# Kernel tuning notes

Measured on AMD Instinct MI355X. Metric: run time of the kernel, lower is better.

Reference implementation:

```python
import jax, jax.numpy as jnp
import numpy as np
import math

B, L, N, DIM, H = 2, 8, 1024, 512, 8
DH = DIM // H

def setup_inputs() -> dict:
    key = jax.random.key(0)
    ks = jax.random.split(key, 9)
    s = 1.0 / math.sqrt(DIM)
    return {
        "x": jax.random.normal(ks[0], (B, L, N, DIM), dtype=jnp.float32),
        "Wq": jax.random.normal(ks[1], (DIM, DIM), dtype=jnp.float32) * s,
        "bq": jnp.zeros((DIM,), dtype=jnp.float32),
        "Wk": jax.random.normal(ks[2], (DIM, DIM), dtype=jnp.float32) * s,
        "bk": jnp.zeros((DIM,), dtype=jnp.float32),
        "Wv": jax.random.normal(ks[3], (DIM, DIM), dtype=jnp.float32) * s,
        "bv": jnp.zeros((DIM,), dtype=jnp.float32),
        "Wo": jax.random.normal(ks[4], (DIM, DIM), dtype=jnp.float32) * s,
        "bo": jnp.zeros((DIM,), dtype=jnp.float32),
    }

def _split_heads(t):
    # 'b l n (h d) -> b l h n d'
    b, l, n, _ = t.shape
    return t.reshape(b, l, n, H, DH).transpose(0, 1, 3, 2, 4)

def reference(x, Wq, bq, Wk, bk, Wv, bv, Wo, bo):
    q = _split_heads(x @ Wq.T + bq)
    # FAITHFUL BUG: source maps (q, v, k) -> (q_mat, k_mat, v_mat),
    # so the "keys" come from the v projection and "values" from the k projection.
    k_mat = _split_heads(x @ Wv.T + bv)
    v_mat = _split_heads(x @ Wk.T + bk)
    # scale is sqrt(Dh * num_heads) = sqrt(dim), as in the source
    scores = jnp.einsum('blhnd,blhmd->blhnm', q, k_mat) / math.sqrt(DIM)
    weights = jax.nn.softmax(scores, axis=-1)
    inter = jnp.einsum('blhnm,blhmd->blhnd', weights, v_mat)
    # 'b l h n d -> b l n (h d)'
    inter = inter.transpose(0, 1, 3, 2, 4).reshape(x.shape[0], x.shape[1], x.shape[2], DIM)
    return inter @ Wo.T + bo
```

## Files before the change

kernel.cpp:

```cpp
#include <hip/hip_runtime.h>
#include <stdint.h>

#define DIMC 512
#define NSEQ 1024
#define BLT  16
#define NHEAD 8
#define DHD  64
#define MTOT (BLT*NSEQ)

typedef float f32x4 __attribute__((ext_vector_type(4)));
typedef short s16x8 __attribute__((ext_vector_type(8)));
typedef short s16x4 __attribute__((ext_vector_type(4)));

__device__ __forceinline__ unsigned short f2bf(float f) {
    unsigned int u = __float_as_uint(f);
    u += 0x7fffu + ((u >> 16) & 1u);
    return (unsigned short)(u >> 16);
}
__device__ __forceinline__ float bf2f(unsigned short h) {
    return __uint_as_float(((unsigned int)h) << 16);
}

#define QSCALE (0.04419417382415922f * 1.4426950408889634f)

__device__ __forceinline__ void gll16(const void* g, void* l) {
    __builtin_amdgcn_global_load_lds(
        (const __attribute__((address_space(1))) void*)g,
        (__attribute__((address_space(3))) void*)l, 16, 0, 0);
}

__device__ __forceinline__ f32x4 mfma16_bf16(s16x4 a, s16x4 b, f32x4 c) {
#if __has_builtin(__builtin_amdgcn_mfma_f32_16x16x16bf16_1k)
    return __builtin_amdgcn_mfma_f32_16x16x16bf16_1k(a, b, c, 0, 0, 0);
#else
    asm volatile("v_mfma_f32_16x16x16_bf16 %0, %1, %2, %0"
                 : "+v"(c) : "v"(a), "v"(b));
    return c;
#endif
}

__device__ __forceinline__ bool detect_bf16(const unsigned short* x) {
    int t = threadIdx.x & 63;
    unsigned short v = x[2 * t];
    int e = (v >> 7) & 0xFF;
    unsigned long long ball = __ballot(e < 100 || e > 137);
    return __popcll(ball) < 16;
}

struct ConvArgs {
    const void* src[9];
    unsigned short* dst[9];
};

__global__ __launch_bounds__(256) void conv_kernel(ConvArgs a,
                                                   const unsigned short* __restrict__ xdet) {
    const bool isbf = detect_bf16(xdet);
    int b = blockIdx.x;
    int seg, idx;
    if (b < 4096)      { seg = 0; idx = (b * 256 + threadIdx.x) * 8; }
    else if (b < 4608) { int t = b - 4096; seg = 1 + (t >> 7);
                         idx = (((t & 127) * 256) + threadIdx.x) * 8; }
    else               { int i = threadIdx.x * 8; seg = 5 + (i >> 9); idx = i & 511; }
    const void* s = a.src[seg];
    unsigned short* d = a.dst[seg];
    if (isbf) {
        *(uint4*)(d + idx) = *(const uint4*)((const unsigned short*)s + idx);
    } else {
        float4 t0 = *(const float4*)((const float*)s + idx);
        float4 t1 = *(const float4*)((const float*)s + idx + 4);
        ushort4 v0{f2bf(t0.x), f2bf(t0.y), f2bf(t0.z), f2bf(t0.w)};
        ushort4 v1{f2bf(t1.x), f2bf(t1.y), f2bf(t1.z), f2bf(t1.w)};
        *(ushort4*)(d + idx)     = v0;
        *(ushort4*)(d + idx + 4) = v1;
    }
}

__device__ __forceinline__ void gemm_core_async(
    const unsigned short* __restrict__ Ap, const unsigned short* __restrict__ Wp,
    int mBase, int nBase, unsigned short* Al, unsigned short* Bl, f32x4 acc[4][4])
{
    const int wave = threadIdx.x >> 6;
    const int lane = threadIdx.x & 63;
    const int lr = lane & 15, lg = lane >> 4;
    const int wm = wave >> 1, wn = wave & 1;
    const int srow = lane >> 3;
    const int scol = (lane & 7) * 8;

    #pragma unroll
    for (int a = 0; a < 4; ++a)
        #pragma unroll
        for (int b = 0; b < 4; ++b) acc[a][b] = (f32x4){0.f, 0.f, 0.f, 0.f};

    for (int k0 = 0; k0 < DIMC; k0 += 64) {
        #pragma unroll
        for (int i = 0; i < 4; ++i) {
            int rbase = (wave * 4 + i) * 8;
            gll16(Ap + (long)(mBase + rbase + srow) * DIMC + k0 + scol, Al + rbase * 64);
            gll16(Wp + (long)(nBase + rbase + srow) * DIMC + k0 + scol, Bl + rbase * 64);
        }
        __syncthreads();

        #pragma unroll
        for (int kk = 0; kk < 64; kk += 32) {
            s16x8 af[4], bf_[4];
            #pragma unroll
            for (int a = 0; a < 4; ++a)
                af[a] = *(const s16x8*)&Al[(wm * 64 + a * 16 + lr) * 64 + kk + lg * 8];
            #pragma unroll
            for (int b = 0; b < 4; ++b)
                bf_[b] = *(const s16x8*)&Bl[(wn * 64 + b * 16 + lr) * 64 + kk + lg * 8];
            #pragma unroll
            for (int a = 0; a < 4; ++a)
                #pragma unroll
                for (int b = 0; b < 4; ++b)
                    acc[a][b] = __builtin_amdgcn_mfma_f32_16x16x32_bf16(af[a], bf_[b], acc[a][b], 0, 0, 0);
        }
        __syncthreads();
    }
}

__global__ __launch_bounds__(256) void proj_kernel(
    const unsigned short* __restrict__ xb,
    const unsigned short* __restrict__ Wqb, const unsigned short* __restrict__ Wkb,
    const unsigned short* __restrict__ Wvb,
    const unsigned short* __restrict__ bqb, const unsigned short* __restrict__ bkb,
    const unsigned short* __restrict__ bvb,
    unsigned short* __restrict__ Q, unsigned short* __restrict__ K,
    unsigned short* __restrict__ Vt)
{
    const int z = blockIdx.z;
    const unsigned short* Wp = (z == 0) ? Wqb : ((z == 1) ? Wvb : Wkb);
    const unsigned short* bp = (z == 0) ? bqb : ((z == 1) ? bvb : bkb);
    unsigned short* outp = (z == 0) ? Q : ((z == 1) ? K : Vt);
    const float oscale = (z == 0) ? QSCALE : 1.0f;

    const int mBase = blockIdx.x * 128;
    const int nBase = blockIdx.y * 128;
    const int lane = threadIdx.x & 63;
    const int lr = lane & 15, lg = lane >> 4;
    const int wm = (threadIdx.x >> 6) >> 1, wn = (threadIdx.x >> 6) & 1;

    __shared__ unsigned short Al[128 * 64];
    __shared__ unsigned short Bl[128 * 64];
    f32x4 acc[4][4];
    gemm_core_async(xb, Wp, mBase, nBase, Al, Bl, acc);

    #pragma unroll
    for (int b = 0; b < 4; ++b) {
        int j = nBase + wn * 64 + b * 16 + lr;
        float bb = bf2f(bp[j]);
        int h = j >> 6, d = j & 63;
        #pragma unroll
        for (int a = 0; a < 4; ++a) {
            int m0 = mBase + wm * 64 + a * 16 + lg * 4;
            int bl = m0 >> 10, n0 = m0 & 1023;
            if (z == 2) {
                ushort4 pk;
                unsigned short* p = (unsigned short*)&pk;
                #pragma unroll
                for (int r = 0; r < 4; ++r) p[r] = f2bf(acc[a][b][r] + bb);
                *(ushort4*)&outp[(((bl << 3) + h) << 16) + (d << 10) + n0] = pk;
            } else {
                #pragma unroll
                for (int r = 0; r < 4; ++r) {
                    float v = (acc[a][b][r] + bb) * oscale;
                    outp[(((bl << 3) + h) << 16) + ((n0 + r) << 6) + d] = f2bf(v);
                }
            }
        }
    }
}

__global__ __launch_bounds__(256) void out_gemm_kernel(
    const unsigned short* __restrict__ inter, const unsigned short* __restrict__ Wob,
    const unsigned short* __restrict__ bob, void* __restrict__ outp,
    const unsigned short* __restrict__ xdet)
{
    const bool isbf = detect_bf16(xdet);
    const int mBase = blockIdx.x * 128;
    const int nBase = blockIdx.y * 128;
    const int lane = threadIdx.x & 63;
    const int lr = lane & 15, lg = lane >> 4;
    const int wm = (threadIdx.x >> 6) >> 1, wn = (threadIdx.x >> 6) & 1;

    __shared__ unsigned short Al[128 * 64];
    __shared__ unsigned short Bl[128 * 64];
    f32x4 acc[4][4];
    gemm_core_async(inter, Wob, mBase, nBase, Al, Bl, acc);

    #pragma unroll
    for (int b = 0; b < 4; ++b) {
        int j = nBase + wn * 64 + b * 16 + lr;
        float bb = bf2f(bob[j]);
        #pragma unroll
        for (int a = 0; a < 4; ++a) {
            #pragma unroll
            for (int r = 0; r < 4; ++r) {
                long m = mBase + wm * 64 + a * 16 + lg * 4 + r;
                float v = acc[a][b][r] + bb;
                if (isbf) ((unsigned short*)outp)[m * DIMC + j] = f2bf(v);
                else      ((float*)outp)[m * DIMC + j] = v;
            }
        }
    }
}

#define SWZ(row, col) ((row) * 64 + ((col) ^ (((row) & 7) * 8)))

__global__ __launch_bounds__(256) void attn_kernel(
    const unsigned short* __restrict__ Q, const unsigned short* __restrict__ K,
    const unsigned short* __restrict__ Vt, unsigned short* __restrict__ inter)
{
    const int inst = blockIdx.x;
    const int bh = inst >> 2;
    const int qt = inst & 3;
    const int wave = threadIdx.x >> 6;
    const int lane = threadIdx.x & 63;
    const int lr = lane & 15;
    const int lg = lane >> 4;

    const unsigned short* Qb = Q + (long)bh * (NSEQ * DHD);
    const int qbase = qt * 256 + wave * 64;

    s16x8 qf[4][2];
    #pragma unroll
    for (int g = 0; g < 4; ++g)
        #pragma unroll
        for (int kk = 0; kk < 2; ++kk)
            qf[g][kk] = *(const s16x8*)&Qb[(qbase + g * 16 + lr) * DHD + kk * 32 + lg * 8];

    __shared__ unsigned short Kl[64 * 64];
    __shared__ unsigned short Vl[64 * 64];

    f32x4 o[4][4];
    #pragma unroll
    for (int g = 0; g < 4; ++g)
        #pragma unroll
        for (int m = 0; m < 4; ++m) o[g][m] = (f32x4){0.f, 0.f, 0.f, 0.f};
    float l_acc[4] = {0.f, 0.f, 0.f, 0.f};

    for (int kt = 0; kt < 16; ++kt) {
        const unsigned short* Kb = K + (long)bh * (NSEQ * DHD) + kt * 64 * DHD;
        const unsigned short* Vb = Vt + (long)bh * (NSEQ * DHD) + kt * 64;

        #pragma unroll
        for (int i = 0; i < 2; ++i) {
            int f = threadIdx.x + 256 * i;
            int row = f >> 3, c8 = (f & 7) * 8;
            *(uint4*)&Kl[SWZ(row, c8)] = *(const uint4*)&Kb[row * DHD + c8];
            *(uint4*)&Vl[SWZ(row, c8)] = *(const uint4*)&Vb[row * NSEQ + c8];
        }
        __syncthreads();

        f32x4 s[4][4];
        #pragma unroll
        for (int g = 0; g < 4; ++g)
            #pragma unroll
            for (int c = 0; c < 4; ++c) s[g][c] = (f32x4){0.f, 0.f, 0.f, 0.f};
        #pragma unroll
        for (int kk = 0; kk < 2; ++kk) {
            s16x8 af[4];
            #pragma unroll
            for (int c = 0; c < 4; ++c)
                af[c] = *(const s16x8*)&Kl[SWZ(c * 16 + lr, kk * 32 + lg * 8)];
            #pragma unroll
            for (int g = 0; g < 4; ++g)
                #pragma unroll
                for (int c = 0; c < 4; ++c)
                    s[g][c] = __builtin_amdgcn_mfma_f32_16x16x32_bf16(af[c], qf[g][kk], s[g][c], 0, 0, 0);
        }

        s16x4 pb[4][4];
        #pragma unroll
        for (int g = 0; g < 4; ++g)
            #pragma unroll
            for (int c = 0; c < 4; ++c) {
                float p0 = __builtin_exp2f(s[g][c][0]);
                float p1 = __builtin_exp2f(s[g][c][1]);
                float p2 = __builtin_exp2f(s[g][c][2]);
                float p3 = __builtin_exp2f(s[g][c][3]);
                l_acc[g] += (p0 + p1) + (p2 + p3);
                unsigned int u0 = __float_as_uint(p0) + 0x8000u;
                unsigned int u1 = __float_as_uint(p1) + 0x8000u;
                unsigned int u2 = __float_as_uint(p2) + 0x8000u;
                unsigned int u3 = __float_as_uint(p3) + 0x8000u;
                union { s16x4 v; unsigned int u[2]; } pk;
                pk.u[0] = __builtin_amdgcn_perm(u1, u0, 0x07060302u);
                pk.u[1] = __builtin_amdgcn_perm(u3, u2, 0x07060302u);
                pb[g][c] = pk.v;
            }

        #pragma unroll
        for (int c = 0; c < 4; ++c) {
            s16x4 va[4];
            #pragma unroll
            for (int m = 0; m < 4; ++m)
                va[m] = *(const s16x4*)&Vl[SWZ(m * 16 + lr, c * 16 + lg * 4)];
            #pragma unroll
            for (int g = 0; g < 4; ++g)
                #pragma unroll
                for (int m = 0; m < 4; ++m)
                    o[g][m] = mfma16_bf16(va[m], pb[g][c], o[g][m]);
        }
        __syncthreads();
    }

    const int bl = bh >> 3, h = bh & 7;
    #pragma unroll
    for (int g = 0; g < 4; ++g) {
        float l = l_acc[g];
        l += __shfl_xor(l, 16);
        l += __shfl_xor(l, 32);
        float inv = 1.f / l;
        const int n = qbase + g * 16 + lr;
        #pragma unroll
        for (int m = 0; m < 4; ++m) {
            ushort4 pk;
            unsigned short* p = (unsigned short*)&pk;
            #pragma unroll
            for (int r = 0; r < 4; ++r) p[r] = f2bf(o[g][m][r] * inv);
            *(ushort4*)&inter[((long)(bl * NSEQ + n)) * DIMC + h * 64 + m * 16 + lg * 4] = pk;
        }
    }
}

extern "C" void kernel_launch(void* const* d_in, const int* in_sizes, int n_in,
                              void* d_out, int out_size, void* d_ws, size_t ws_size,
                              hipStream_t stream) {
    const void* x  = d_in[0];
    const void* Wq = d_in[1]; const void* bq = d_in[2];
    const void* Wk = d_in[3]; const void* bk = d_in[4];
    const void* Wv = d_in[5]; const void* bv = d_in[6];
    const void* Wo = d_in[7]; const void* bo = d_in[8];

    char* ws = (char*)d_ws;
    unsigned short* xb  = (unsigned short*)ws;
    unsigned short* Q   = xb + (long)MTOT * DIMC;
    unsigned short* K   = Q  + (long)MTOT * DIMC;
    unsigned short* Vt  = K  + (long)MTOT * DIMC;
    unsigned short* Wqb = Vt + (long)MTOT * DIMC;
    unsigned short* Wkb = Wqb + DIMC * DIMC;
    unsigned short* Wvb = Wkb + DIMC * DIMC;
    unsigned short* Wob = Wvb + DIMC * DIMC;
    unsigned short* bqb = Wob + DIMC * DIMC;
    unsigned short* bkb = bqb + DIMC;
    unsigned short* bvb = bkb + DIMC;
    unsigned short* bob = bvb + DIMC;

    ConvArgs ca;
    ca.src[0] = x;  ca.src[1] = Wq; ca.src[2] = Wk; ca.src[3] = Wv; ca.src[4] = Wo;
    ca.src[5] = bq; ca.src[6] = bk; ca.src[7] = bv; ca.src[8] = bo;
    ca.dst[0] = xb;  ca.dst[1] = Wqb; ca.dst[2] = Wkb; ca.dst[3] = Wvb; ca.dst[4] = Wob;
    ca.dst[5] = bqb; ca.dst[6] = bkb; ca.dst[7] = bvb; ca.dst[8] = bob;
    conv_kernel<<<4609, 256, 0, stream>>>(ca, (const unsigned short*)x);

    dim3 gp(MTOT / 128, DIMC / 128, 3);
    proj_kernel<<<gp, 256, 0, stream>>>(xb, Wqb, Wkb, Wvb, bqb, bkb, bvb, Q, K, Vt);

    attn_kernel<<<BLT * NHEAD * 4, 256, 0, stream>>>(Q, K, Vt, xb );

    dim3 go(MTOT / 128, DIMC / 128);
    out_gemm_kernel<<<go, 256, 0, stream>>>(xb , Wob, bob, d_out,
                                            (const unsigned short*)x);
}
```

Before: 241.6 us.

## Load K/V fragments straight from global memory and halve per-block query tile

```diff
diff --git a/kernel.cpp b/kernel.cpp
--- a/kernel.cpp
+++ b/kernel.cpp
@@ -205,74 +205,62 @@
     }
 }
 
-#define SWZ(row, col) ((row) * 64 + ((col) ^ (((row) & 7) * 8)))
-
 __global__ __launch_bounds__(256) void attn_kernel(
     const unsigned short* __restrict__ Q, const unsigned short* __restrict__ K,
     const unsigned short* __restrict__ Vt, unsigned short* __restrict__ inter)
 {
-    const int inst = blockIdx.x;
-    const int bh = inst >> 2;
-    const int qt = inst & 3;
+    const int b = blockIdx.x;
+    const int bh = b & 127;
+    const int qt = b >> 7;
     const int wave = threadIdx.x >> 6;
     const int lane = threadIdx.x & 63;
     const int lr = lane & 15;
     const int lg = lane >> 4;
 
     const unsigned short* Qb = Q + (long)bh * (NSEQ * DHD);
-    const int qbase = qt * 256 + wave * 64;
-
-    s16x8 qf[4][2];
-    #pragma unroll
-    for (int g = 0; g < 4; ++g)
+    const unsigned short* Kb = K + (long)bh * (NSEQ * DHD);
+    const unsigned short* Vb = Vt + (long)bh * (NSEQ * DHD);
+    const int qbase = qt * 128 + wave * 32;
+
+    s16x8 qf[2][2];
+    #pragma unroll
+    for (int g = 0; g < 2; ++g)
         #pragma unroll
         for (int kk = 0; kk < 2; ++kk)
             qf[g][kk] = *(const s16x8*)&Qb[(qbase + g * 16 + lr) * DHD + kk * 32 + lg * 8];
 
-    __shared__ unsigned short Kl[64 * 64];
-    __shared__ unsigned short Vl[64 * 64];
-
-    f32x4 o[4][4];
-    #pragma unroll
-    for (int g = 0; g < 4; ++g)
+    f32x4 o[2][4];
+    #pragma unroll
+    for (int g = 0; g < 2; ++g)
         #pragma unroll
         for (int m = 0; m < 4; ++m) o[g][m] = (f32x4){0.f, 0.f, 0.f, 0.f};
-    float l_acc[4] = {0.f, 0.f, 0.f, 0.f};
-
+    float l_acc[2] = {0.f, 0.f};
+
+    #pragma unroll 2
     for (int kt = 0; kt < 16; ++kt) {
-        const unsigned short* Kb = K + (long)bh * (NSEQ * DHD) + kt * 64 * DHD;
-        const unsigned short* Vb = Vt + (long)bh * (NSEQ * DHD) + kt * 64;
-
-        #pragma unroll
-        for (int i = 0; i < 2; ++i) {
-            int f = threadIdx.x + 256 * i;
-            int row = f >> 3, c8 = (f & 7) * 8;
-            *(uint4*)&Kl[SWZ(row, c8)] = *(const uint4*)&Kb[row * DHD + c8];
-            *(uint4*)&Vl[SWZ(row, c8)] = *(const uint4*)&Vb[row * NSEQ + c8];
-        }
-        __syncthreads();
-
-        f32x4 s[4][4];
-        #pragma unroll
-        for (int g = 0; g < 4; ++g)
+        s16x8 af[2][4];
+        #pragma unroll
+        for (int kk = 0; kk < 2; ++kk)
+            #pragma unroll
+            for (int c = 0; c < 4; ++c)
+                af[kk][c] = *(const s16x8*)&Kb[(kt * 64 + c * 16 + lr) * DHD + kk * 32 + lg * 8];
+
+        f32x4 s[2][4];
+        #pragma unroll
+        for (int g = 0; g < 2; ++g)
             #pragma unroll
             for (int c = 0; c < 4; ++c) s[g][c] = (f32x4){0.f, 0.f, 0.f, 0.f};
         #pragma unroll
-        for (int kk = 0; kk < 2; ++kk) {
-            s16x8 af[4];
-            #pragma unroll
-            for (int c = 0; c < 4; ++c)
-                af[c] = *(const s16x8*)&Kl[SWZ(c * 16 + lr, kk * 32 + lg * 8)];
-            #pragma unroll
-            for (int g = 0; g < 4; ++g)
+        for (int kk = 0; kk < 2; ++kk)
+            #pragma unroll
+            for (int g = 0; g < 2; ++g)
                 #pragma unroll
                 for (int c = 0; c < 4; ++c)
-                    s[g][c] = __builtin_amdgcn_mfma_f32_16x16x32_bf16(af[c], qf[g][kk], s[g][c], 0, 0, 0);
-        }
-
-        s16x4 pb[4][4];
-        #pragma unroll
-        for (int g = 0; g < 4; ++g)
+                    s[g][c] = __builtin_amdgcn_mfma_f32_16x16x32_bf16(af[kk][c], qf[g][kk], s[g][c], 0, 0, 0);
+
+        s16x4 pb[2][4];
+        #pragma unroll
+        for (int g = 0; g < 2; ++g)
             #pragma unroll
             for (int c = 0; c < 4; ++c) {
                 float p0 = __builtin_exp2f(s[g][c][0]);
@@ -295,19 +283,18 @@
             s16x4 va[4];
             #pragma unroll
             for (int m = 0; m < 4; ++m)
-                va[m] = *(const s16x4*)&Vl[SWZ(m * 16 + lr, c * 16 + lg * 4)];
-            #pragma unroll
-            for (int g = 0; g < 4; ++g)
+                va[m] = *(const s16x4*)&Vb[(m * 16 + lr) * NSEQ + kt * 64 + c * 16 + lg * 4];
+            #pragma unroll
+            for (int g = 0; g < 2; ++g)
                 #pragma unroll
                 for (int m = 0; m < 4; ++m)
                     o[g][m] = mfma16_bf16(va[m], pb[g][c], o[g][m]);
         }
-        __syncthreads();
     }
 
     const int bl = bh >> 3, h = bh & 7;
     #pragma unroll
-    for (int g = 0; g < 4; ++g) {
+    for (int g = 0; g < 2; ++g) {
         float l = l_acc[g];
         l += __shfl_xor(l, 16);
         l += __shfl_xor(l, 32);
@@ -357,7 +344,7 @@
     dim3 gp(MTOT / 128, DIMC / 128, 3);
     proj_kernel<<<gp, 256, 0, stream>>>(xb, Wqb, Wkb, Wvb, bqb, bkb, bvb, Q, K, Vt);
 
-    attn_kernel<<<BLT * NHEAD * 4, 256, 0, stream>>>(Q, K, Vt, xb );
+    attn_kernel<<<8 * 128, 256, 0, stream>>>(Q, K, Vt, xb );
 
     dim3 go(MTOT / 128, DIMC / 128);
     out_gemm_kernel<<<go, 256, 0, stream>>>(xb , Wob, bob, d_out,
```

Result: slower. 338.1 us (+39.9%).
